# Optimization experiments

Hardware: AMD Instinct MI355X
Metric: run time of the kernel (lower is better)

The kernel has to match this reference:

```python
import jax, jax.numpy as jnp
import numpy as np

B, H, W, C = 8, 64, 64, 256
C8 = C // 8  # query/key channels


def setup_inputs() -> dict:
    key = jax.random.key(0)
    ks = jax.random.split(key, 8)
    s = 0.02  # init scale for weights
    return {
        "x": jax.random.normal(ks[0], (B, H, W, C), dtype=jnp.float32),
        "Wq": jax.random.normal(ks[1], (C, C8), dtype=jnp.float32) * s,
        "bq": jnp.zeros((C8,), dtype=jnp.float32),
        "Wk": jax.random.normal(ks[2], (C, C8), dtype=jnp.float32) * s,
        "bk": jnp.zeros((C8,), dtype=jnp.float32),
        "Wv": jax.random.normal(ks[3], (C, C), dtype=jnp.float32) * s,
        "bv": jnp.zeros((C,), dtype=jnp.float32),
        "gamma": jnp.full((1,), 0.5, dtype=jnp.float32),
    }


def reference(x, Wq, bq, Wk, bk, Wv, bv, gamma):
    Bn, Hn, Wn, Cn = x.shape
    N = Hn * Wn
    xf = x.reshape(Bn, N, Cn)            # flatten spatial dims: [B, N, C]
    # 1x1 convs == per-pixel dense projections over channels
    q = xf @ Wq + bq                     # [B, N, C//8]
    k = xf @ Wk + bk                     # [B, N, C//8]
    v = xf @ Wv + bv                     # [B, N, C]
    # energy[b,i,j] = k_i . q_j  (matches tf.matmul(key, query, transpose_b=True))
    energy = jnp.einsum('bic,bjc->bij', k, q)   # [B, N, N]
    attn = jax.nn.softmax(energy, axis=-1)      # softmax over last axis
    # out_i = sum_j attn[i,j] * v_j  (intended SAGAN aggregation in NHWC layout)
    out = jnp.einsum('bij,bjc->bic', attn, v)   # [B, N, C]
    out = out.reshape(Bn, Hn, Wn, Cn)
    return gamma * out + x
```

## Files before the change

kernel.cpp:

```cpp
#include <hip/hip_runtime.h>

typedef __attribute__((ext_vector_type(8))) short short8;
typedef __attribute__((ext_vector_type(4))) float f32x4;
typedef __attribute__((ext_vector_type(16))) float f32x16;
typedef __attribute__((ext_vector_type(2))) unsigned int u32x2;
typedef __attribute__((ext_vector_type(4))) unsigned int u32x4;
typedef unsigned short u16;
typedef unsigned int u32;

#define MFMA16(a, b, c) __builtin_amdgcn_mfma_f32_16x16x32_bf16((a), (b), (c), 0, 0, 0)
#define MFMA32(a, b, c) __builtin_amdgcn_mfma_f32_32x32x16_bf16((a), (b), (c), 0, 0, 0)

#define BAR_VMEM() asm volatile("s_waitcnt vmcnt(0) lgkmcnt(0)\ns_barrier" ::: "memory")
#define BAR_LDS()  asm volatile("s_waitcnt lgkmcnt(0)\ns_barrier" ::: "memory")

#define BATCH 8
#define NTOK 4096
#define CDIM 256
#define CQK 32
#define LOG2E 1.4426950408889634f

__device__ __forceinline__ u16 f2bf(float f) {
  u32 u = __float_as_uint(f);
  return (u16)((u + 0x7FFFu + ((u >> 16) & 1u)) >> 16);
}
__device__ __forceinline__ u32 pack2(float a, float b) {
  const u32 ua = __float_as_uint(a) + 0x8000u;
  const u32 ub = __float_as_uint(b) + 0x8000u;
#if __has_builtin(__builtin_amdgcn_perm)
  return __builtin_amdgcn_perm(ub, ua, 0x07060302u);
#else
  return (ua >> 16) | (ub & 0xFFFF0000u);
#endif
}
__device__ __forceinline__ float fexp2(float x) {
#if __has_builtin(__builtin_amdgcn_exp2f)
  return __builtin_amdgcn_exp2f(x);
#else
  return exp2f(x);
#endif
}
__device__ __forceinline__ void gl_lds16(const u16* g, u16* l) {
  __builtin_amdgcn_global_load_lds(
      (const __attribute__((address_space(1))) unsigned int*)(g),
      (__attribute__((address_space(3))) unsigned int*)(l), 16, 0, 0);
}

__global__ void k_prep(const float* __restrict__ Wq, const float* __restrict__ bq,
                       const float* __restrict__ Wk, const float* __restrict__ bk,
                       const float* __restrict__ Wv, const float* __restrict__ bv,
                       u16* __restrict__ wtf, float* __restrict__ bias) {
  const int f = blockIdx.x;
  const int L = threadIdx.x;
  const int ct = f >> 3, ks = f & 7;
  const int o = ct * 16 + (L & 15);
  const int ch = ks * 32 + (L >> 4) * 8;
  short8 v8;
#pragma unroll
  for (int jj = 0; jj < 8; jj++) {
    const int c = ch + jj;
    float v;
    if (o < 32)       v = Wq[c * CQK + o];
    else if (o < 64)  v = Wk[c * CQK + (o - 32)];
    else              v = Wv[c * CDIM + (o - 64)];
    v8[jj] = (short)f2bf(v);
  }
  *(short8*)(wtf + (size_t)f * 512 + L * 8) = v8;
  if (f == 0) {
    for (int i = L; i < 320; i += 64) {
      if (i < 32)      bias[i] = bq[i];
      else if (i < 64) bias[i] = bk[i - 32];
      else             bias[i] = bv[i - 64];
    }
  }
}

__global__ __launch_bounds__(256, 2) void k_proj(
    const float* __restrict__ x, const u16* __restrict__ wtf,
    const float* __restrict__ bias,
    u16* __restrict__ q_ws, u16* __restrict__ k_ws, u16* __restrict__ vt_ws) {
  __shared__ u16 x_lds[64 * 264];
  __shared__ u16 vt_t[64 * 72];
  const int m0 = blockIdx.x * 64;
  const int tid = threadIdx.x;
  const int w = tid >> 6, L = tid & 63;
  const int lr = L & 15, q4 = L >> 4;

  short8 wfA[5], wfB[5];
#pragma unroll
  for (int j = 0; j < 5; j++)
    wfA[j] = *(const short8*)(wtf + ((size_t)((j * 4 + w) * 8 + 0)) * 512 + L * 8);

#pragma unroll
  for (int ii = 0; ii < 8; ii++) {
    const int e = (tid + 256 * ii) * 8;
    const int row = e >> 8, col = e & 255;
    const float* src = x + (size_t)(m0 + row) * CDIM + col;
    f32x4 a = *(const f32x4*)src;
    f32x4 b4 = *(const f32x4*)(src + 4);
    u32x4 pk;
    pk[0] = pack2(a[0], a[1]);
    pk[1] = pack2(a[2], a[3]);
    pk[2] = pack2(b4[0], b4[1]);
    pk[3] = pack2(b4[2], b4[3]);
    *(u32x4*)&x_lds[row * 264 + col] = pk;
  }
  __syncthreads();

  f32x4 acc[4][5];
#pragma unroll
  for (int rg = 0; rg < 4; rg++)
#pragma unroll
    for (int j = 0; j < 5; j++) acc[rg][j] = (f32x4){0.f, 0.f, 0.f, 0.f};

#pragma unroll
  for (int ks = 0; ks < 8; ks++) {
    if (ks < 7) {
#pragma unroll
      for (int j = 0; j < 5; j++) {
        short8 v = *(const short8*)(wtf +
            ((size_t)((j * 4 + w) * 8 + ks + 1)) * 512 + L * 8);
        if (ks & 1) wfA[j] = v; else wfB[j] = v;
      }
    }
#pragma unroll
    for (int rg = 0; rg < 4; rg++) {
      short8 a = *(const short8*)&x_lds[(rg * 16 + lr) * 264 + ks * 32 + q4 * 8];
#pragma unroll
      for (int j = 0; j < 5; j++)
        acc[rg][j] = MFMA16(a, (ks & 1) ? wfB[j] : wfA[j], acc[rg][j]);
    }
  }

  {
    const float bb = bias[w * 16 + lr];
#pragma unroll
    for (int rg = 0; rg < 4; rg++)
#pragma unroll
      for (int r = 0; r < 4; r++) {
        const int row = m0 + rg * 16 + q4 * 4 + r;
        float v = acc[rg][0][r] + bb;
        if (w < 2) q_ws[(size_t)row * CQK + w * 16 + lr] = f2bf(v);
        else       k_ws[(size_t)row * CQK + (w - 2) * 16 + lr] = f2bf(v * LOG2E);
      }
  }
  const int b = m0 >> 12, nloc = m0 & 4095;
  const int rb2 = ((lr >> 3) & 1) << 2;
  const int c_l = w * 16 + lr;
#pragma unroll
  for (int cg = 0; cg < 4; cg++) {
    __syncthreads();
    const int j = cg + 1;
    const float bb = bias[(4 + cg * 4 + w) * 16 + lr];
#pragma unroll
    for (int rg = 0; rg < 4; rg++) {
      const int n_base = (rg * 16 + q4 * 4) ^ rb2;
      u32x2 pk;
      pk[0] = pack2(acc[rg][j][0] + bb, acc[rg][j][1] + bb);
      pk[1] = pack2(acc[rg][j][2] + bb, acc[rg][j][3] + bb);
      *(u32x2*)&vt_t[c_l * 72 + n_base] = pk;
    }
    __syncthreads();
#pragma unroll
    for (int i = 0; i < 2; i++) {
      const int gch = tid + 256 * i;
      const int cl2 = gch >> 3, jc = gch & 7;
      short8 v = *(const short8*)&vt_t[cl2 * 72 + jc * 8];
      *(short8*)(vt_ws + ((size_t)(b * CDIM + cg * 64 + cl2)) * NTOK + nloc + jc * 8) = v;
    }
  }
}

__global__ __launch_bounds__(256, 4) void k_attn(
    const float* __restrict__ x, const u16* __restrict__ q_ws,
    const u16* __restrict__ k_ws, const u16* __restrict__ vt_ws,
    const float* __restrict__ gamma, float* __restrict__ out) {
  __shared__ u16 vt_lds[2][128 * 64];
  __shared__ u16 p_lds[64 * 64];

  const int bid = blockIdx.x;
  const int b = bid & 7;
  const int chalf = (bid >> 3) & 1;
  const int it = bid >> 4;
  const int i0 = it * 64;
  const int c0 = chalf * 128;
  const int tid = threadIdx.x;
  const int w = tid >> 6, L = tid & 63;
  const int lr = L & 15, q4 = L >> 4;
  const int L31 = L & 31, Lhi = L >> 5, L7 = L & 7;
  const int ih = w & 1, cpair = w >> 1;

  const short8 a_k = *(const short8*)(k_ws +
      ((size_t)(b * NTOK + i0 + w * 16 + lr)) * CQK + q4 * 8);

  const int cl_base = tid >> 3;
  const int jc_sw = (tid & 7) ^ (cl_base & 7);
  const u16* vt_g = vt_ws + ((size_t)(b * CDIM + c0 + cl_base)) * NTOK + jc_sw * 8;
  const u16* q_base = q_ws + (size_t)b * NTOK * CQK;

  f32x16 o_acc[2];
#pragma unroll
  for (int t = 0; t < 2; t++)
#pragma unroll
    for (int e = 0; e < 16; e++) o_acc[t][e] = 0.f;
  float lsum = 0.f;

  u16* pw0 = p_lds + (w * 16 + lr) * 64 + (((q4 & 1) ^ ((lr >> 3) & 1)) << 2);
  const int q4h = q4 >> 1;

  short8 bqA[4], bqB[4];
#pragma unroll
  for (int t = 0; t < 4; t++)
    bqA[t] = *(const short8*)(q_base + (size_t)(t * 16 + lr) * CQK + q4 * 8);
#pragma unroll
  for (int ii = 0; ii < 4; ii++)
    gl_lds16(vt_g + (size_t)(ii * 32) * NTOK, &vt_lds[0][ii * 2048 + w * 512]);

#define ATTN_ITER(JT, VB_CUR, VB_NXT, BQ, BQN)                                   \
  do {                                                                           \
    const int j0 = (JT) * 64;                                                    \
    BAR_LDS();                         \
       \
    _Pragma("unroll")                                                            \
    for (int t = 0; t < 4; t++)                                                  \
      BQN[t] = *(const short8*)(q_base +                                         \
               (size_t)(j0 + 64 + t * 16 + lr) * CQK + q4 * 8);                  \
                  \
    f32x4 s[4];                                                                  \
    _Pragma("unroll")                                                            \
    for (int t = 0; t < 4; t++)                                                  \
      s[t] = MFMA16(BQ[t], a_k, ((f32x4){0.f, 0.f, 0.f, 0.f}));                  \
                   \
    _Pragma("unroll")                                                            \
    for (int t = 0; t < 4; t++) {                                                \
      const float p0 = fexp2(s[t][0]);                                           \
      const float p1 = fexp2(s[t][1]);                                           \
      const float p2 = fexp2(s[t][2]);                                           \
      const float p3 = fexp2(s[t][3]);                                           \
      lsum += (p0 + p1) + (p2 + p3);                                             \
      u32x2 pk;                                                                  \
      pk[0] = pack2(p0, p1);                                                     \
      pk[1] = pack2(p2, p3);                                                     \
      *(u32x2*)(pw0 + (((2 * t + q4h) ^ (lr & 7)) * 8)) = pk;                    \
    }                                                                            \
    BAR_VMEM();          \
              \
    if ((JT) < 63) {                                                             \
      _Pragma("unroll")                                                          \
      for (int ii = 0; ii < 4; ii++)                                             \
        gl_lds16(vt_g + (size_t)(ii * 32) * NTOK + (j0 + 64),                    \
                 &VB_NXT[ii * 2048 + w * 512]);                                  \
    }                                                                            \
            \
    _Pragma("unroll")                                                            \
    for (int ks = 0; ks < 4; ks++) {                                             \
      const int slot = (((ks * 2 + Lhi) ^ L7)) * 8;                              \
      short8 a_p = *(const short8*)(p_lds + (ih * 32 + L31) * 64 + slot);        \
      _Pragma("unroll")                                                          \
      for (int ct2 = 0; ct2 < 2; ct2++) {                                        \
        const int cl = (cpair * 2 + ct2) * 32 + L31;                             \
        short8 b_v = *(const short8*)(&VB_CUR[0] + cl * 64 + slot);              \
        o_acc[ct2] = MFMA32(a_p, b_v, o_acc[ct2]);                               \
      }                                                                          \
    }                                                                            \
  } while (0)

  for (int jt2 = 0; jt2 < 64; jt2 += 2) {
    ATTN_ITER(jt2,     vt_lds[0], vt_lds[1], bqA, bqB);
    ATTN_ITER(jt2 + 1, vt_lds[1], vt_lds[0], bqB, bqA);
  }
#undef ATTN_ITER

  float s2 = lsum;
  s2 += __shfl_xor(s2, 16);
  s2 += __shfl_xor(s2, 32);
  const float rl = 1.0f / s2;
  BAR_LDS();
  float* lp = (float*)p_lds;
  if (q4 == 0) lp[w * 16 + lr] = rl;
  BAR_LDS();

  float linv[16];
#pragma unroll
  for (int rg = 0; rg < 16; rg++)
    linv[rg] = lp[ih * 32 + (rg & 3) + 8 * (rg >> 2) + 4 * Lhi];

  const float g = gamma[0];
#pragma unroll
  for (int ct2 = 0; ct2 < 2; ct2++) {
    const int c = c0 + (cpair * 2 + ct2) * 32 + L31;
#pragma unroll
    for (int rg = 0; rg < 16; rg++) {
      const int i = i0 + ih * 32 + (rg & 3) + 8 * (rg >> 2) + 4 * Lhi;
      const size_t idx = ((size_t)(b * NTOK + i)) * CDIM + c;
      out[idx] = g * (o_acc[ct2][rg] * linv[rg]) + x[idx];
    }
  }
}

extern "C" void kernel_launch(void* const* d_in, const int* in_sizes, int n_in,
                              void* d_out, int out_size, void* d_ws, size_t ws_size,
                              hipStream_t stream) {
  const float* x  = (const float*)d_in[0];
  const float* Wq = (const float*)d_in[1];
  const float* bq = (const float*)d_in[2];
  const float* Wk = (const float*)d_in[3];
  const float* bk = (const float*)d_in[4];
  const float* Wv = (const float*)d_in[5];
  const float* bv = (const float*)d_in[6];
  const float* gamma = (const float*)d_in[7];
  float* out = (float*)d_out;

  char* ws = (char*)d_ws;
  u16* q_ws  = (u16*)(ws);
  u16* k_ws  = (u16*)(ws + (2u << 20));
  u16* vt_ws = (u16*)(ws + (4u << 20));
  u16* wtf   = (u16*)(ws + (20u << 20));
  float* bias = (float*)(ws + (20u << 20) + (256u << 10));

  k_prep<<<160, 64, 0, stream>>>(Wq, bq, Wk, bk, Wv, bv, wtf, bias);
  k_proj<<<512, 256, 0, stream>>>(x, wtf, bias, q_ws, k_ws, vt_ws);
  k_attn<<<1024, 256, 0, stream>>>(x, q_ws, k_ws, vt_ws, gamma, out);
}
```

Measured before the change: 214.1 us.

## Compute all 256 channels per attention block to avoid duplicate score work

Each attention block now covers the full 256-channel output instead of half, which halves the grid to 512 blocks. The QK^T scores and exp/softmax computation, previously repeated by two blocks per query tile, is now done once. Each wave reuses its P fragments across two row halves of a doubled V tile in LDS. The next-tile Q prefetch also moves after the V load issue. The cost is double the LDS V buffer (64KB), more accumulator registers, launch bounds of 2 blocks per SM, and fewer blocks to fill the device.

```diff
diff --git a/kernel.cpp b/kernel.cpp
--- a/kernel.cpp
+++ b/kernel.cpp
@@ -171,38 +171,37 @@
   }
 }
 
-__global__ __launch_bounds__(256, 4) void k_attn(
+__global__ __launch_bounds__(256, 2) void k_attn(
     const float* __restrict__ x, const u16* __restrict__ q_ws,
     const u16* __restrict__ k_ws, const u16* __restrict__ vt_ws,
     const float* __restrict__ gamma, float* __restrict__ out) {
-  __shared__ u16 vt_lds[2][128 * 64];
+  __shared__ u16 vt_lds[2][256 * 64];
   __shared__ u16 p_lds[64 * 64];
 
   const int bid = blockIdx.x;
   const int b = bid & 7;
-  const int chalf = (bid >> 3) & 1;
-  const int it = bid >> 4;
+  const int it = bid >> 3;
   const int i0 = it * 64;
-  const int c0 = chalf * 128;
   const int tid = threadIdx.x;
   const int w = tid >> 6, L = tid & 63;
   const int lr = L & 15, q4 = L >> 4;
   const int L31 = L & 31, Lhi = L >> 5, L7 = L & 7;
-  const int ih = w & 1, cpair = w >> 1;
 
   const short8 a_k = *(const short8*)(k_ws +
       ((size_t)(b * NTOK + i0 + w * 16 + lr)) * CQK + q4 * 8);
 
   const int cl_base = tid >> 3;
   const int jc_sw = (tid & 7) ^ (cl_base & 7);
-  const u16* vt_g = vt_ws + ((size_t)(b * CDIM + c0 + cl_base)) * NTOK + jc_sw * 8;
+  const u16* vt_g = vt_ws + ((size_t)(b * CDIM + cl_base)) * NTOK + jc_sw * 8;
   const u16* q_base = q_ws + (size_t)b * NTOK * CQK;
 
-  f32x16 o_acc[2];
-#pragma unroll
-  for (int t = 0; t < 2; t++)
-#pragma unroll
-    for (int e = 0; e < 16; e++) o_acc[t][e] = 0.f;
+  f32x16 o_acc[2][2];
+#pragma unroll
+  for (int ih = 0; ih < 2; ih++)
+#pragma unroll
+    for (int ct2 = 0; ct2 < 2; ct2++)
+#pragma unroll
+      for (int e = 0; e < 16; e++) o_acc[ih][ct2][e] = 0.f;
   float lsum = 0.f;
 
   u16* pw0 = p_lds + (w * 16 + lr) * 64 + (((q4 & 1) ^ ((lr >> 3) & 1)) << 2);
@@ -213,19 +212,14 @@
   for (int t = 0; t < 4; t++)
     bqA[t] = *(const short8*)(q_base + (size_t)(t * 16 + lr) * CQK + q4 * 8);
 #pragma unroll
-  for (int ii = 0; ii < 4; ii++)
+  for (int ii = 0; ii < 8; ii++)
     gl_lds16(vt_g + (size_t)(ii * 32) * NTOK, &vt_lds[0][ii * 2048 + w * 512]);
 
 #define ATTN_ITER(JT, VB_CUR, VB_NXT, BQ, BQN)                                   \
   do {                                                                           \
     const int j0 = (JT) * 64;                                                    \
     BAR_LDS();                         \
-       \
-    _Pragma("unroll")                                                            \
-    for (int t = 0; t < 4; t++)                                                  \
-      BQN[t] = *(const short8*)(q_base +                                         \
-               (size_t)(j0 + 64 + t * 16 + lr) * CQK + q4 * 8);                  \
-                  \
+                             \
     f32x4 s[4];                                                                  \
     _Pragma("unroll")                                                            \
     for (int t = 0; t < 4; t++)                                                  \
@@ -244,23 +238,29 @@
       *(u32x2*)(pw0 + (((2 * t + q4h) ^ (lr & 7)) * 8)) = pk;                    \
     }                                                                            \
     BAR_VMEM();          \
-              \
+             \
     if ((JT) < 63) {                                                             \
       _Pragma("unroll")                                                          \
-      for (int ii = 0; ii < 4; ii++)                                             \
+      for (int ii = 0; ii < 8; ii++)                                             \
         gl_lds16(vt_g + (size_t)(ii * 32) * NTOK + (j0 + 64),                    \
                  &VB_NXT[ii * 2048 + w * 512]);                                  \
     }                                                                            \
-            \
+    _Pragma("unroll")                                                            \
+    for (int t = 0; t < 4; t++)                                                  \
+      BQN[t] = *(const short8*)(q_base +                                         \
+               (size_t)(j0 + 64 + t * 16 + lr) * CQK + q4 * 8);                  \
+             \
     _Pragma("unroll")                                                            \
     for (int ks = 0; ks < 4; ks++) {                                             \
       const int slot = (((ks * 2 + Lhi) ^ L7)) * 8;                              \
-      short8 a_p = *(const short8*)(p_lds + (ih * 32 + L31) * 64 + slot);        \
+      short8 a_p0 = *(const short8*)(p_lds + L31 * 64 + slot);                   \
+      short8 a_p1 = *(const short8*)(p_lds + (32 + L31) * 64 + slot);            \
       _Pragma("unroll")                                                          \
       for (int ct2 = 0; ct2 < 2; ct2++) {                                        \
-        const int cl = (cpair * 2 + ct2) * 32 + L31;                             \
-        short8 b_v = *(const short8*)(&VB_CUR[0] + cl * 64 + slot);              \
-        o_acc[ct2] = MFMA32(a_p, b_v, o_acc[ct2]);                               \
+        const int cl = w * 64 + ct2 * 32 + L31;                                  \
+        short8 b_v = *(const short8*)(VB_CUR + cl * 64 + slot);                  \
+        o_acc[0][ct2] = MFMA32(a_p0, b_v, o_acc[0][ct2]);                        \
+        o_acc[1][ct2] = MFMA32(a_p1, b_v, o_acc[1][ct2]);                        \
       }                                                                          \
     }                                                                            \
   } while (0)
@@ -280,22 +280,26 @@
   if (q4 == 0) lp[w * 16 + lr] = rl;
   BAR_LDS();
 
-  float linv[16];
-#pragma unroll
-  for (int rg = 0; rg < 16; rg++)
-    linv[rg] = lp[ih * 32 + (rg & 3) + 8 * (rg >> 2) + 4 * Lhi];
+  float linv2[2][16];
+#pragma unroll
+  for (int ih = 0; ih < 2; ih++)
+#pragma unroll
+    for (int rg = 0; rg < 16; rg++)
+      linv2[ih][rg] = lp[ih * 32 + (rg & 3) + 8 * (rg >> 2) + 4 * Lhi];
 
   const float g = gamma[0];
 #pragma unroll
-  for (int ct2 = 0; ct2 < 2; ct2++) {
-    const int c = c0 + (cpair * 2 + ct2) * 32 + L31;
-#pragma unroll
-    for (int rg = 0; rg < 16; rg++) {
-      const int i = i0 + ih * 32 + (rg & 3) + 8 * (rg >> 2) + 4 * Lhi;
-      const size_t idx = ((size_t)(b * NTOK + i)) * CDIM + c;
-      out[idx] = g * (o_acc[ct2][rg] * linv[rg]) + x[idx];
-    }
-  }
+  for (int ih = 0; ih < 2; ih++)
+#pragma unroll
+    for (int ct2 = 0; ct2 < 2; ct2++) {
+      const int c = w * 64 + ct2 * 32 + L31;
+#pragma unroll
+      for (int rg = 0; rg < 16; rg++) {
+        const int i = i0 + ih * 32 + (rg & 3) + 8 * (rg >> 2) + 4 * Lhi;
+        const size_t idx = ((size_t)(b * NTOK + i)) * CDIM + c;
+        out[idx] = g * (o_acc[ih][ct2][rg] * linv2[ih][rg]) + x[idx];
+      }
+    }
 }
 
 extern "C" void kernel_launch(void* const* d_in, const int* in_sizes, int n_in,
@@ -320,5 +324,5 @@
 
   k_prep<<<160, 64, 0, stream>>>(Wq, bq, Wk, bk, Wv, bv, wtf, bias);
   k_proj<<<512, 256, 0, stream>>>(x, wtf, bias, q_ws, k_ws, vt_ws);
-  k_attn<<<1024, 256, 0, stream>>>(x, q_ws, k_ws, vt_ws, gamma, out);
-}
+  k_attn<<<512, 256, 0, stream>>>(x, q_ws, k_ws, vt_ws, gamma, out);
+}
```

After: 196.8 us. 1.09x faster.
